# Kernel optimization log

Hardware: AMD Instinct MI355X
Metric: run time of the kernel (lower is better)

The kernel has to match this reference:

```python
import jax, jax.numpy as jnp
import numpy as np

H = 16  # num_heads (from init_kwargs)


def setup_inputs() -> dict:
    key = jax.random.key(0)
    ks = jax.random.split(key, 12)
    B, S, E = 4, 1024, 1024
    inp = {
        "query": jax.random.normal(ks[0], (B, S, E), jnp.float32),
        "key": jax.random.normal(ks[1], (B, S, E), jnp.float32),
        "value": jax.random.normal(ks[2], (B, S, E), jnp.float32),
        "mask": jax.random.randint(ks[3], (B, S, S), 0, 2, jnp.int32),
        # nn.Linear params: y = x @ W.T + b
        "Wq": jax.random.normal(ks[4], (E, E), jnp.float32) * 0.02,
        "bq": jnp.zeros((E,), jnp.float32),
        "Wk": jax.random.normal(ks[5], (E, E), jnp.float32) * 0.02,
        "bk": jnp.zeros((E,), jnp.float32),
        "Wv": jax.random.normal(ks[6], (E, E), jnp.float32) * 0.02,
        "bv": jnp.zeros((E,), jnp.float32),
        "Wo": jax.random.normal(ks[7], (E, E), jnp.float32) * 0.02,
        "bo": jnp.zeros((E,), jnp.float32),
    }
    return inp


def reference(query, key, value, mask, Wq, bq, Wk, bk, Wv, bv, Wo, bo):
    # Dropout treated as identity (eval mode) for a deterministic baseline.
    B, Sq, E = query.shape
    Sk = key.shape[1]
    D = E // H
    scale = jnp.sqrt(jnp.float32(D))

    Q = (query @ Wq.T + bq).reshape(B, Sq, H, D).transpose(0, 2, 1, 3)  # bhqd
    K = (key @ Wk.T + bk).reshape(B, Sk, H, D).transpose(0, 2, 1, 3)    # bhkd
    V = (value @ Wv.T + bv).reshape(B, Sk, H, D).transpose(0, 2, 1, 3)  # bhkd

    scores = jnp.einsum("bhqd,bhkd->bhqk", Q, K) / scale
    scores = jnp.where(mask[:, None, :, :] == 0, jnp.float32(-1e9), scores)
    attn = jax.nn.softmax(scores, axis=-1)  # [B,H,Sq,Sk]

    ctx = jnp.einsum("bhqk,bhkd->bhqd", attn, V)
    ctx = ctx.transpose(0, 2, 1, 3).reshape(B, Sq, E)
    out = ctx @ Wo.T + bo
    attn_avg = attn.mean(axis=1)  # [B,Sq,Sk]
    return out, attn_avg
```

## Files before the change

kernel.cpp:

```cpp
#include <hip/hip_runtime.h>
#include <hip/hip_bf16.h>
#include <stdint.h>

#define BATCH 4
#define SEQ   1024
#define EMB   1024
#define NH    16
#define HD    64

typedef short s8v __attribute__((ext_vector_type(8)));
typedef float f4v __attribute__((ext_vector_type(4)));

__device__ __forceinline__ uint16_t f2bf(float f) {
    __hip_bfloat16 h = __float2bfloat16(f);
    return *reinterpret_cast<uint16_t*>(&h);
}
__device__ __forceinline__ short bfraw(float f) {
    __hip_bfloat16 h = __float2bfloat16(f);
    return *reinterpret_cast<short*>(&h);
}
__device__ __forceinline__ s8v cvt8(const float* p) {
    float4 a = *(const float4*)p;
    float4 b = *(const float4*)(p + 4);
    s8v r;
    r[0] = bfraw(a.x); r[1] = bfraw(a.y); r[2] = bfraw(a.z); r[3] = bfraw(a.w);
    r[4] = bfraw(b.x); r[5] = bfraw(b.y); r[6] = bfraw(b.z); r[7] = bfraw(b.w);
    return r;
}

__global__ __launch_bounds__(256) void pack_mask(
        const int* __restrict__ mask, unsigned long long* __restrict__ Mb64)
{
    const size_t gid = (size_t)blockIdx.x * 256 + threadIdx.x;
    const unsigned long long bal = __ballot(mask[gid] != 0);
    if ((threadIdx.x & 63) == 0) Mb64[gid >> 6] = bal;
}

__global__ __launch_bounds__(256) void cvt_all(
        const float* __restrict__ W0, const float* __restrict__ W1,
        const float* __restrict__ W2, const float* __restrict__ W3,
        const float* __restrict__ X0, const float* __restrict__ X1,
        const float* __restrict__ X2,
        uint16_t* __restrict__ Wdst, uint16_t* __restrict__ Xq,
        uint16_t* __restrict__ Xk, uint16_t* __restrict__ Xv)
{
    const int y = blockIdx.y;
    const size_t off = ((size_t)blockIdx.x * 256 + threadIdx.x) * 8;
    if (y < 4) {
        if (blockIdx.x >= 512) return;
        const float* s = (y == 0) ? W0 : (y == 1) ? W1 : (y == 2) ? W2 : W3;
        *(s8v*)(Wdst + (size_t)y * EMB * EMB + off) = cvt8(s + off);
    } else {
        const float* s = (y == 4) ? X0 : (y == 5) ? X1 : X2;
        uint16_t*    d = (y == 4) ? Xq : (y == 5) ? Xk : Xv;
        *(s8v*)(d + off) = cvt8(s + off);
    }
}

__global__ __launch_bounds__(512, 2) void gemm3(
        const uint16_t* __restrict__ X0, const uint16_t* __restrict__ W0,
        const float* __restrict__ b0, void* __restrict__ o0, int sc0, float ss0,
        const uint16_t* __restrict__ X1, const uint16_t* __restrict__ W1,
        const float* __restrict__ b1, void* __restrict__ o1, int sc1, float ss1,
        const uint16_t* __restrict__ X2, const uint16_t* __restrict__ W2,
        const float* __restrict__ b2, void* __restrict__ o2, int sc2, float ss2)
{
    __shared__ __attribute__((aligned(16))) uint16_t As[128][40];
    __shared__ __attribute__((aligned(16))) uint16_t Bs[128][40];

    const int z = blockIdx.z;
    const uint16_t* Xb   = (z == 0) ? X0 : (z == 1) ? X1 : X2;
    const uint16_t* Wb   = (z == 0) ? W0 : (z == 1) ? W1 : W2;
    const float*    bias = (z == 0) ? b0 : (z == 1) ? b1 : b2;
    void*           outv = (z == 0) ? o0 : (z == 1) ? o1 : o2;
    const int     scatter = (z == 0) ? sc0 : (z == 1) ? sc1 : sc2;
    const float   scale   = (z == 0) ? ss0 : (z == 1) ? ss1 : ss2;

    const int t    = threadIdx.x;
    const int lane = t & 63;
    const int w    = t >> 6;
    const int wm = w & 1;
    const int wn = w >> 1;
    const int m0 = blockIdx.y * 128;
    const int n0 = blockIdx.x * 128;
    const int ar = lane & 15;
    const int aq = lane >> 4;

    const int srow = t >> 2;
    const int scol = (t & 3) * 8;

    const uint16_t* gA = Xb + (size_t)(m0 + srow) * EMB + scol;
    const uint16_t* gB = Wb + (size_t)(n0 + srow) * EMB + scol;

    f4v acc[4][2];
    #pragma unroll
    for (int i = 0; i < 4; ++i)
        #pragma unroll
        for (int j = 0; j < 2; ++j) acc[i][j] = (f4v){0.f, 0.f, 0.f, 0.f};

    s8v ra = *(const s8v*)gA;
    s8v rb = *(const s8v*)gB;

    for (int k0 = 0; k0 < EMB; k0 += 32) {
        __syncthreads();
        *(s8v*)&As[srow][scol] = ra;
        *(s8v*)&Bs[srow][scol] = rb;
        const int kn = (k0 + 32) & (EMB - 1);
        ra = *(const s8v*)(gA + kn);
        rb = *(const s8v*)(gB + kn);
        __syncthreads();

        s8v af[4], bf[2];
        #pragma unroll
        for (int i = 0; i < 4; ++i)
            af[i] = *(const s8v*)&As[wm * 64 + i * 16 + ar][aq * 8];
        #pragma unroll
        for (int j = 0; j < 2; ++j)
            bf[j] = *(const s8v*)&Bs[wn * 32 + j * 16 + ar][aq * 8];
        #pragma unroll
        for (int i = 0; i < 4; ++i)
            #pragma unroll
            for (int j = 0; j < 2; ++j)
                acc[i][j] = __builtin_amdgcn_mfma_f32_16x16x32_bf16(af[i], bf[j], acc[i][j], 0, 0, 0);
    }

    #pragma unroll
    for (int i = 0; i < 4; ++i) {
        const int crow = m0 + wm * 64 + i * 16 + aq * 4;
        #pragma unroll
        for (int j = 0; j < 2; ++j) {
            const int n = n0 + wn * 32 + j * 16 + ar;
            const float bv = bias[n];
            #pragma unroll
            for (int r = 0; r < 4; ++r) {
                const int m = crow + r;
                const float v = (acc[i][j][r] + bv) * scale;
                if (scatter == 1) {
                    size_t idx = (size_t)(((m >> 10) * NH + (n >> 6)) * SEQ + (m & 1023)) * HD + (n & 63);
                    ((uint16_t*)outv)[idx] = f2bf(v);
                } else if (scatter == 2) {
                    size_t idx = (size_t)(((m >> 10) * NH + (n >> 6)) * HD + (n & 63)) * SEQ + (m & 1023);
                    ((uint16_t*)outv)[idx] = f2bf(v);
                } else {
                    ((float*)outv)[(size_t)m * EMB + n] = v;
                }
            }
        }
    }
}

__global__ __launch_bounds__(256, 4) void flash_ctx(
        const uint16_t* __restrict__ Qb, const uint16_t* __restrict__ Kb,
        const uint16_t* __restrict__ Vt, const uint32_t* __restrict__ Mb,
        uint16_t* __restrict__ ctx, float* __restrict__ linv_out)
{
    __shared__ uint32_t Ml[4][16][33];
    __shared__ __attribute__((aligned(16))) uint16_t Pt[4][2][16][56];

    const int t = threadIdx.x;
    const int w = t >> 6, lane = t & 63;
    const int ar = lane & 15, aq = lane >> 4;

    const int id   = blockIdx.x;
    const int xcd  = id & 7;
    const int rest = id >> 3;
    const int bh   = xcd * 8 + (rest & 7);
    const int qt   = (rest >> 3) * 4 + w;
    const int b = bh >> 4, h = bh & 15;
    const size_t hb = ((size_t)(b * NH + h)) * SEQ * HD;

    {
        const uint32_t* src = Mb + (((size_t)b * SEQ + qt * 16) << 5);
        uint4 m0 = *(const uint4*)(src + lane * 8);
        uint4 m1 = *(const uint4*)(src + lane * 8 + 4);
        const int pr = (lane * 8) >> 5, pc = (lane * 8) & 31;
        Ml[w][pr][pc + 0] = m0.x; Ml[w][pr][pc + 1] = m0.y;
        Ml[w][pr][pc + 2] = m0.z; Ml[w][pr][pc + 3] = m0.w;
        Ml[w][pr][pc + 4] = m1.x; Ml[w][pr][pc + 5] = m1.y;
        Ml[w][pr][pc + 6] = m1.z; Ml[w][pr][pc + 7] = m1.w;
    }

    const uint16_t* qp = Qb + hb + (size_t)(qt * 16 + ar) * HD + aq * 8;
    const s8v a0 = *(const s8v*)qp;
    const s8v a1 = *(const s8v*)(qp + 32);

    const uint16_t* kbase = Kb + hb + (size_t)ar * HD + aq * 8;
    const uint16_t* vbase = Vt + hb + (size_t)ar * SEQ + aq * 8;

    f4v OA0 = {0.f,0.f,0.f,0.f}, OA1 = OA0, OA2 = OA0, OA3 = OA0;
    f4v OB0 = OA0, OB1 = OA0, OB2 = OA0, OB3 = OA0;
    float lsA[4] = {0.f, 0.f, 0.f, 0.f};
    float lsB[4] = {0.f, 0.f, 0.f, 0.f};

    for (int ci = 0; ci < 16; ++ci) {
        const int cA = ci * 2, cB = ci * 2 + 1;
        const int kcA = cA * 32, kcB = cB * 32;

        const uint16_t* kA = kbase + (size_t)kcA * HD;
        const uint16_t* kB = kbase + (size_t)kcB * HD;
        s8v Abl0 = *(const s8v*)kA,            Abh0 = *(const s8v*)(kA + 32);
        s8v Abl1 = *(const s8v*)(kA + 16*HD),  Abh1 = *(const s8v*)(kA + 16*HD + 32);
        s8v Bbl0 = *(const s8v*)kB,            Bbh0 = *(const s8v*)(kB + 32);
        s8v Bbl1 = *(const s8v*)(kB + 16*HD),  Bbh1 = *(const s8v*)(kB + 16*HD + 32);

        f4v z = {0.f,0.f,0.f,0.f};
        f4v sA0 = __builtin_amdgcn_mfma_f32_16x16x32_bf16(a0, Abl0, z, 0, 0, 0);
        sA0 = __builtin_amdgcn_mfma_f32_16x16x32_bf16(a1, Abh0, sA0, 0, 0, 0);
        f4v sA1 = __builtin_amdgcn_mfma_f32_16x16x32_bf16(a0, Abl1, z, 0, 0, 0);
        sA1 = __builtin_amdgcn_mfma_f32_16x16x32_bf16(a1, Abh1, sA1, 0, 0, 0);
        f4v sB0 = __builtin_amdgcn_mfma_f32_16x16x32_bf16(a0, Bbl0, z, 0, 0, 0);
        sB0 = __builtin_amdgcn_mfma_f32_16x16x32_bf16(a1, Bbh0, sB0, 0, 0, 0);
        f4v sB1 = __builtin_amdgcn_mfma_f32_16x16x32_bf16(a0, Bbl1, z, 0, 0, 0);
        sB1 = __builtin_amdgcn_mfma_f32_16x16x32_bf16(a1, Bbh1, sB1, 0, 0, 0);

        const uint16_t* vA = vbase + kcA;
        const uint16_t* vB = vbase + kcB;
        s8v Av0 = *(const s8v*)(vA);
        s8v Av1 = *(const s8v*)(vA + 16 * SEQ);
        s8v Av2 = *(const s8v*)(vA + 32 * SEQ);
        s8v Av3 = *(const s8v*)(vA + 48 * SEQ);
        s8v Bv0 = *(const s8v*)(vB);
        s8v Bv1 = *(const s8v*)(vB + 16 * SEQ);
        s8v Bv2 = *(const s8v*)(vB + 32 * SEQ);
        s8v Bv3 = *(const s8v*)(vB + 48 * SEQ);

        #pragma unroll
        for (int r = 0; r < 4; ++r) {
            const uint32_t mwA = Ml[w][aq * 4 + r][cA];
            const float e0 = ((mwA >> ar) & 1u)        ? __expf(sA0[r]) : 0.f;
            const float e1 = ((mwA >> (16 + ar)) & 1u) ? __expf(sA1[r]) : 0.f;
            lsA[r] += e0 + e1;
            Pt[w][0][aq * 4 + r][ar]      = f2bf(e0);
            Pt[w][0][aq * 4 + r][16 + ar] = f2bf(e1);
        }
        #pragma unroll
        for (int r = 0; r < 4; ++r) {
            const uint32_t mwB = Ml[w][aq * 4 + r][cB];
            const float e0 = ((mwB >> ar) & 1u)        ? __expf(sB0[r]) : 0.f;
            const float e1 = ((mwB >> (16 + ar)) & 1u) ? __expf(sB1[r]) : 0.f;
            lsB[r] += e0 + e1;
            Pt[w][1][aq * 4 + r][ar]      = f2bf(e0);
            Pt[w][1][aq * 4 + r][16 + ar] = f2bf(e1);
        }

        const s8v paA = *(const s8v*)&Pt[w][0][ar][aq * 8];
        OA0 = __builtin_amdgcn_mfma_f32_16x16x32_bf16(paA, Av0, OA0, 0, 0, 0);
        OA1 = __builtin_amdgcn_mfma_f32_16x16x32_bf16(paA, Av1, OA1, 0, 0, 0);
        OA2 = __builtin_amdgcn_mfma_f32_16x16x32_bf16(paA, Av2, OA2, 0, 0, 0);
        OA3 = __builtin_amdgcn_mfma_f32_16x16x32_bf16(paA, Av3, OA3, 0, 0, 0);
        const s8v paB = *(const s8v*)&Pt[w][1][ar][aq * 8];
        OB0 = __builtin_amdgcn_mfma_f32_16x16x32_bf16(paB, Bv0, OB0, 0, 0, 0);
        OB1 = __builtin_amdgcn_mfma_f32_16x16x32_bf16(paB, Bv1, OB1, 0, 0, 0);
        OB2 = __builtin_amdgcn_mfma_f32_16x16x32_bf16(paB, Bv2, OB2, 0, 0, 0);
        OB3 = __builtin_amdgcn_mfma_f32_16x16x32_bf16(paB, Bv3, OB3, 0, 0, 0);
    }

    float lsum[4];
    #pragma unroll
    for (int r = 0; r < 4; ++r) {
        OA0[r] += OB0[r]; OA1[r] += OB1[r];
        OA2[r] += OB2[r]; OA3[r] += OB3[r];
        lsum[r] = lsA[r] + lsB[r];
    }

    #pragma unroll
    for (int off = 1; off < 16; off <<= 1) {
        #pragma unroll
        for (int r = 0; r < 4; ++r) lsum[r] += __shfl_xor(lsum[r], off);
    }
    float inv[4];
    #pragma unroll
    for (int r = 0; r < 4; ++r) inv[r] = 1.0f / lsum[r];

    #pragma unroll
    for (int r = 0; r < 4; ++r) {
        const int q = qt * 16 + aq * 4 + r;
        uint16_t* cp = ctx + ((size_t)(b * SEQ + q) * NH + h) * HD + ar;
        cp[ 0] = f2bf(OA0[r] * inv[r]);
        cp[16] = f2bf(OA1[r] * inv[r]);
        cp[32] = f2bf(OA2[r] * inv[r]);
        cp[48] = f2bf(OA3[r] * inv[r]);
    }
    if (ar == 0) {
        #pragma unroll
        for (int r = 0; r < 4; ++r)
            linv_out[(size_t)(b * NH + h) * SEQ + qt * 16 + aq * 4 + r] = inv[r];
    }
}

__global__ __launch_bounds__(512, 4) void attn_avg(
        const uint16_t* __restrict__ Qb, const uint16_t* __restrict__ Kb,
        const uint32_t* __restrict__ Mb, const float* __restrict__ linv,
        float* __restrict__ attn_out)
{
    const int qt = blockIdx.x;
    const int b  = blockIdx.y >> 2;
    const int kq = blockIdx.y & 3;
    const int t = threadIdx.x;
    const int w = t >> 6, lane = t & 63;
    const int ar = lane & 15, aq = lane >> 4;
    const int k0 = kq * 256 + w * 32;

    uint32_t mw[4];
    #pragma unroll
    for (int r = 0; r < 4; ++r)
        mw[r] = Mb[(((size_t)b * SEQ + qt * 16 + aq * 4 + r) << 5) + (k0 >> 5)];

    float acc[8];
    #pragma unroll
    for (int j = 0; j < 8; ++j) acc[j] = 0.f;

    for (int h = 0; h < NH; ++h) {
        const size_t hb = ((size_t)(b * NH + h)) * SEQ * HD;
        const uint16_t* qp = Qb + hb + (size_t)(qt * 16 + ar) * HD + aq * 8;
        const s8v a0 = *(const s8v*)qp;
        const s8v a1 = *(const s8v*)(qp + 32);
        float fs[4];
        #pragma unroll
        for (int r = 0; r < 4; ++r)
            fs[r] = linv[(size_t)(b * NH + h) * SEQ + qt * 16 + aq * 4 + r] * 0.0625f;

        #pragma unroll
        for (int nt = 0; nt < 2; ++nt) {
            const uint16_t* kp = Kb + hb + (size_t)(k0 + nt * 16 + ar) * HD + aq * 8;
            s8v bl = *(const s8v*)kp, bh2 = *(const s8v*)(kp + 32);
            f4v z = {0.f,0.f,0.f,0.f};
            f4v s = __builtin_amdgcn_mfma_f32_16x16x32_bf16(a0, bl, z, 0, 0, 0);
            s = __builtin_amdgcn_mfma_f32_16x16x32_bf16(a1, bh2, s, 0, 0, 0);
            #pragma unroll
            for (int r = 0; r < 4; ++r) {
                const int bit = nt * 16 + ar;
                if ((mw[r] >> bit) & 1u) acc[r * 2 + nt] += __expf(s[r]) * fs[r];
            }
        }
    }

    #pragma unroll
    for (int r = 0; r < 4; ++r) {
        float* ap = attn_out + ((size_t)b * SEQ + qt * 16 + aq * 4 + r) * SEQ + k0 + ar;
        #pragma unroll
        for (int nt = 0; nt < 2; ++nt) ap[nt * 16] = acc[r * 2 + nt];
    }
}

extern "C" void kernel_launch(void* const* d_in, const int* in_sizes, int n_in,
                              void* d_out, int out_size, void* d_ws, size_t ws_size,
                              hipStream_t stream) {
    const float* q_in = (const float*)d_in[0];
    const float* k_in = (const float*)d_in[1];
    const float* v_in = (const float*)d_in[2];
    const int*   mask = (const int*)d_in[3];
    const float* Wq = (const float*)d_in[4];
    const float* bq = (const float*)d_in[5];
    const float* Wk = (const float*)d_in[6];
    const float* bk = (const float*)d_in[7];
    const float* Wv = (const float*)d_in[8];
    const float* bv = (const float*)d_in[9];
    const float* Wo = (const float*)d_in[10];
    const float* bo = (const float*)d_in[11];

    float* out      = (float*)d_out;
    float* attn_out = out + (size_t)BATCH * SEQ * EMB;

    const size_t qkv_elems = (size_t)BATCH * NH * SEQ * HD;
    uint16_t* Qb  = (uint16_t*)d_ws;
    uint16_t* Kb  = Qb + qkv_elems;
    uint16_t* Vt  = Kb + qkv_elems;
    uint16_t* ctx = Vt + qkv_elems;
    uint16_t* Wcb = ctx + (size_t)BATCH * SEQ * EMB;
    uint16_t* Wqb = Wcb;
    uint16_t* Wkb = Wcb + (size_t)EMB * EMB;
    uint16_t* Wvb = Wcb + 2 * (size_t)EMB * EMB;
    uint16_t* Wob = Wcb + 3 * (size_t)EMB * EMB;
    uint16_t* Xq  = Wcb + 4 * (size_t)EMB * EMB;
    uint16_t* Xk  = Xq + qkv_elems;
    uint16_t* Xv  = ctx;
    uint32_t* Mb32 = (uint32_t*)(Xk + qkv_elems);
    float*    linv = (float*)(Mb32 + (size_t)BATCH * SEQ * 32);

    pack_mask<<<dim3((BATCH * SEQ * SEQ) / 256), 256, 0, stream>>>(
        mask, (unsigned long long*)Mb32);
    cvt_all<<<dim3(2048, 7), 256, 0, stream>>>(Wq, Wk, Wv, Wo, q_in, k_in, v_in,
                                               Wcb, Xq, Xk, Xv);

    dim3 g3(EMB / 128, (BATCH * SEQ) / 128, 3);
    gemm3<<<g3, 512, 0, stream>>>(
        Xq, Wqb, bq, Qb, 1, 0.125f,
        Xk, Wkb, bk, Kb, 1, 1.0f,
        Xv, Wvb, bv, Vt, 2, 1.0f);

    flash_ctx<<<dim3(1024), 256, 0, stream>>>(Qb, Kb, Vt, Mb32, ctx, linv);
    attn_avg<<<dim3(SEQ / 16, BATCH * 4), 512, 0, stream>>>(Qb, Kb, Mb32, linv, attn_out);

    dim3 g1(EMB / 128, (BATCH * SEQ) / 128, 1);
    gemm3<<<g1, 512, 0, stream>>>(
        ctx, Wob, bo, out, 0, 1.0f,
        ctx, Wob, bo, out, 0, 1.0f,
        ctx, Wob, bo, out, 0, 1.0f);
}
```

Baseline: 408.6 us.

## Deepen GEMM K-tile and software-pipeline K/V loads in flash attention

The projection GEMM now stages a 64-wide K slice per iteration, with each thread loading two rows, which halves the number of barrier pairs. The next tile's global loads are issued after the LDS stores and fenced with a sched_barrier. The flash attention kernel replaces its two-chunk interleaved loop with a single-chunk body that double-buffers the K and V registers, prefetching the next chunk before the current compute. This drops the duplicate accumulators and halves the Pt buffer. The gain relies on hiding global load latency, at the cost of more registers and LDS in the GEMM.

Measured after the change: 442.1 us. 8.2% more time.

```diff
diff --git a/kernel.cpp b/kernel.cpp
--- a/kernel.cpp
+++ b/kernel.cpp
@@ -65,8 +65,8 @@
         const uint16_t* __restrict__ X2, const uint16_t* __restrict__ W2,
         const float* __restrict__ b2, void* __restrict__ o2, int sc2, float ss2)
 {
-    __shared__ __attribute__((aligned(16))) uint16_t As[128][40];
-    __shared__ __attribute__((aligned(16))) uint16_t Bs[128][40];
+    __shared__ __attribute__((aligned(16))) uint16_t As[128][72];
+    __shared__ __attribute__((aligned(16))) uint16_t Bs[128][72];
 
     const int z = blockIdx.z;
     const uint16_t* Xb   = (z == 0) ? X0 : (z == 1) ? X1 : X2;
@@ -86,8 +86,8 @@
     const int ar = lane & 15;
     const int aq = lane >> 4;
 
-    const int srow = t >> 2;
-    const int scol = (t & 3) * 8;
+    const int srow = t >> 3;
+    const int scol = (t & 7) * 8;
 
     const uint16_t* gA = Xb + (size_t)(m0 + srow) * EMB + scol;
     const uint16_t* gB = Wb + (size_t)(n0 + srow) * EMB + scol;
@@ -98,30 +98,41 @@
         #pragma unroll
         for (int j = 0; j < 2; ++j) acc[i][j] = (f4v){0.f, 0.f, 0.f, 0.f};
 
-    s8v ra = *(const s8v*)gA;
-    s8v rb = *(const s8v*)gB;
-
-    for (int k0 = 0; k0 < EMB; k0 += 32) {
+    s8v ra0 = *(const s8v*)gA;
+    s8v ra1 = *(const s8v*)(gA + 64 * EMB);
+    s8v rb0 = *(const s8v*)gB;
+    s8v rb1 = *(const s8v*)(gB + 64 * EMB);
+
+    for (int k0 = 0; k0 < EMB; k0 += 64) {
         __syncthreads();
-        *(s8v*)&As[srow][scol] = ra;
-        *(s8v*)&Bs[srow][scol] = rb;
-        const int kn = (k0 + 32) & (EMB - 1);
-        ra = *(const s8v*)(gA + kn);
-        rb = *(const s8v*)(gB + kn);
+        *(s8v*)&As[srow][scol]      = ra0;
+        *(s8v*)&As[srow + 64][scol] = ra1;
+        *(s8v*)&Bs[srow][scol]      = rb0;
+        *(s8v*)&Bs[srow + 64][scol] = rb1;
         __syncthreads();
 
-        s8v af[4], bf[2];
-        #pragma unroll
-        for (int i = 0; i < 4; ++i)
-            af[i] = *(const s8v*)&As[wm * 64 + i * 16 + ar][aq * 8];
-        #pragma unroll
-        for (int j = 0; j < 2; ++j)
-            bf[j] = *(const s8v*)&Bs[wn * 32 + j * 16 + ar][aq * 8];
-        #pragma unroll
-        for (int i = 0; i < 4; ++i)
+        const int kn = (k0 + 64) & (EMB - 1);
+        ra0 = *(const s8v*)(gA + kn);
+        ra1 = *(const s8v*)(gA + 64 * EMB + kn);
+        rb0 = *(const s8v*)(gB + kn);
+        rb1 = *(const s8v*)(gB + 64 * EMB + kn);
+        __builtin_amdgcn_sched_barrier(0);
+
+        #pragma unroll
+        for (int kk = 0; kk < 2; ++kk) {
+            s8v af[4], bf[2];
+            #pragma unroll
+            for (int i = 0; i < 4; ++i)
+                af[i] = *(const s8v*)&As[wm * 64 + i * 16 + ar][kk * 32 + aq * 8];
             #pragma unroll
             for (int j = 0; j < 2; ++j)
-                acc[i][j] = __builtin_amdgcn_mfma_f32_16x16x32_bf16(af[i], bf[j], acc[i][j], 0, 0, 0);
+                bf[j] = *(const s8v*)&Bs[wn * 32 + j * 16 + ar][kk * 32 + aq * 8];
+            #pragma unroll
+            for (int i = 0; i < 4; ++i)
+                #pragma unroll
+                for (int j = 0; j < 2; ++j)
+                    acc[i][j] = __builtin_amdgcn_mfma_f32_16x16x32_bf16(af[i], bf[j], acc[i][j], 0, 0, 0);
+        }
     }
 
     #pragma unroll
@@ -155,7 +166,7 @@
         uint16_t* __restrict__ ctx, float* __restrict__ linv_out)
 {
     __shared__ uint32_t Ml[4][16][33];
-    __shared__ __attribute__((aligned(16))) uint16_t Pt[4][2][16][56];
+    __shared__ __attribute__((aligned(16))) uint16_t Pt[4][16][56];
 
     const int t = threadIdx.x;
     const int w = t >> 6, lane = t & 63;
@@ -187,80 +198,59 @@
     const uint16_t* kbase = Kb + hb + (size_t)ar * HD + aq * 8;
     const uint16_t* vbase = Vt + hb + (size_t)ar * SEQ + aq * 8;
 
-    f4v OA0 = {0.f,0.f,0.f,0.f}, OA1 = OA0, OA2 = OA0, OA3 = OA0;
-    f4v OB0 = OA0, OB1 = OA0, OB2 = OA0, OB3 = OA0;
-    float lsA[4] = {0.f, 0.f, 0.f, 0.f};
-    float lsB[4] = {0.f, 0.f, 0.f, 0.f};
-
-    for (int ci = 0; ci < 16; ++ci) {
-        const int cA = ci * 2, cB = ci * 2 + 1;
-        const int kcA = cA * 32, kcB = cB * 32;
-
-        const uint16_t* kA = kbase + (size_t)kcA * HD;
-        const uint16_t* kB = kbase + (size_t)kcB * HD;
-        s8v Abl0 = *(const s8v*)kA,            Abh0 = *(const s8v*)(kA + 32);
-        s8v Abl1 = *(const s8v*)(kA + 16*HD),  Abh1 = *(const s8v*)(kA + 16*HD + 32);
-        s8v Bbl0 = *(const s8v*)kB,            Bbh0 = *(const s8v*)(kB + 32);
-        s8v Bbl1 = *(const s8v*)(kB + 16*HD),  Bbh1 = *(const s8v*)(kB + 16*HD + 32);
+    f4v O0 = {0.f,0.f,0.f,0.f}, O1 = O0, O2 = O0, O3 = O0;
+    float lsum[4] = {0.f, 0.f, 0.f, 0.f};
+
+    auto body = [&](int ci, s8v* curK, s8v* curV, s8v* nxtK, s8v* nxtV) {
+        const int kcn = ((ci + 1) & 31) * 32;
+        const uint16_t* kn = kbase + (size_t)kcn * HD;
+        const uint16_t* vn = vbase + kcn;
+        nxtK[0] = *(const s8v*)kn;
+        nxtK[1] = *(const s8v*)(kn + 32);
+        nxtK[2] = *(const s8v*)(kn + 16 * HD);
+        nxtK[3] = *(const s8v*)(kn + 16 * HD + 32);
+        nxtV[0] = *(const s8v*)vn;
+        nxtV[1] = *(const s8v*)(vn + 16 * SEQ);
+        nxtV[2] = *(const s8v*)(vn + 32 * SEQ);
+        nxtV[3] = *(const s8v*)(vn + 48 * SEQ);
+        __builtin_amdgcn_sched_barrier(0);
 
         f4v z = {0.f,0.f,0.f,0.f};
-        f4v sA0 = __builtin_amdgcn_mfma_f32_16x16x32_bf16(a0, Abl0, z, 0, 0, 0);
-        sA0 = __builtin_amdgcn_mfma_f32_16x16x32_bf16(a1, Abh0, sA0, 0, 0, 0);
-        f4v sA1 = __builtin_amdgcn_mfma_f32_16x16x32_bf16(a0, Abl1, z, 0, 0, 0);
-        sA1 = __builtin_amdgcn_mfma_f32_16x16x32_bf16(a1, Abh1, sA1, 0, 0, 0);
-        f4v sB0 = __builtin_amdgcn_mfma_f32_16x16x32_bf16(a0, Bbl0, z, 0, 0, 0);
-        sB0 = __builtin_amdgcn_mfma_f32_16x16x32_bf16(a1, Bbh0, sB0, 0, 0, 0);
-        f4v sB1 = __builtin_amdgcn_mfma_f32_16x16x32_bf16(a0, Bbl1, z, 0, 0, 0);
-        sB1 = __builtin_amdgcn_mfma_f32_16x16x32_bf16(a1, Bbh1, sB1, 0, 0, 0);
-
-        const uint16_t* vA = vbase + kcA;
-        const uint16_t* vB = vbase + kcB;
-        s8v Av0 = *(const s8v*)(vA);
-        s8v Av1 = *(const s8v*)(vA + 16 * SEQ);
-        s8v Av2 = *(const s8v*)(vA + 32 * SEQ);
-        s8v Av3 = *(const s8v*)(vA + 48 * SEQ);
-        s8v Bv0 = *(const s8v*)(vB);
-        s8v Bv1 = *(const s8v*)(vB + 16 * SEQ);
-        s8v Bv2 = *(const s8v*)(vB + 32 * SEQ);
-        s8v Bv3 = *(const s8v*)(vB + 48 * SEQ);
+        f4v s0 = __builtin_amdgcn_mfma_f32_16x16x32_bf16(a0, curK[0], z, 0, 0, 0);
+        s0 = __builtin_amdgcn_mfma_f32_16x16x32_bf16(a1, curK[1], s0, 0, 0, 0);
+        f4v s1 = __builtin_amdgcn_mfma_f32_16x16x32_bf16(a0, curK[2], z, 0, 0, 0);
+        s1 = __builtin_amdgcn_mfma_f32_16x16x32_bf16(a1, curK[3], s1, 0, 0, 0);
 
         #pragma unroll
         for (int r = 0; r < 4; ++r) {
-            const uint32_t mwA = Ml[w][aq * 4 + r][cA];
-            const float e0 = ((mwA >> ar) & 1u)        ? __expf(sA0[r]) : 0.f;
-            const float e1 = ((mwA >> (16 + ar)) & 1u) ? __expf(sA1[r]) : 0.f;
-            lsA[r] += e0 + e1;
-            Pt[w][0][aq * 4 + r][ar]      = f2bf(e0);
-            Pt[w][0][aq * 4 + r][16 + ar] = f2bf(e1);
+            const uint32_t mw = Ml[w][aq * 4 + r][ci];
+            const float e0 = ((mw >> ar) & 1u)        ? __expf(s0[r]) : 0.f;
+            const float e1 = ((mw >> (16 + ar)) & 1u) ? __expf(s1[r]) : 0.f;
+            lsum[r] += e0 + e1;
+            Pt[w][aq * 4 + r][ar]      = f2bf(e0);
+            Pt[w][aq * 4 + r][16 + ar] = f2bf(e1);
         }
-        #pragma unroll
-        for (int r = 0; r < 4; ++r) {
-            const uint32_t mwB = Ml[w][aq * 4 + r][cB];
-            const float e0 = ((mwB >> ar) & 1u)        ? __expf(sB0[r]) : 0.f;
-            const float e1 = ((mwB >> (16 + ar)) & 1u) ? __expf(sB1[r]) : 0.f;
-            lsB[r] += e0 + e1;
-            Pt[w][1][aq * 4 + r][ar]      = f2bf(e0);
-            Pt[w][1][aq * 4 + r][16 + ar] = f2bf(e1);
-        }
-
-        const s8v paA = *(const s8v*)&Pt[w][0][ar][aq * 8];
-        OA0 = __builtin_amdgcn_mfma_f32_16x16x32_bf16(paA, Av0, OA0, 0, 0, 0);
-        OA1 = __builtin_amdgcn_mfma_f32_16x16x32_bf16(paA, Av1, OA1, 0, 0, 0);
-        OA2 = __builtin_amdgcn_mfma_f32_16x16x32_bf16(paA, Av2, OA2, 0, 0, 0);
-        OA3 = __builtin_amdgcn_mfma_f32_16x16x32_bf16(paA, Av3, OA3, 0, 0, 0);
-        const s8v paB = *(const s8v*)&Pt[w][1][ar][aq * 8];
-        OB0 = __builtin_amdgcn_mfma_f32_16x16x32_bf16(paB, Bv0, OB0, 0, 0, 0);
-        OB1 = __builtin_amdgcn_mfma_f32_16x16x32_bf16(paB, Bv1, OB1, 0, 0, 0);
-        OB2 = __builtin_amdgcn_mfma_f32_16x16x32_bf16(paB, Bv2, OB2, 0, 0, 0);
-        OB3 = __builtin_amdgcn_mfma_f32_16x16x32_bf16(paB, Bv3, OB3, 0, 0, 0);
-    }
-
-    float lsum[4];
-    #pragma unroll
-    for (int r = 0; r < 4; ++r) {
-        OA0[r] += OB0[r]; OA1[r] += OB1[r];
-        OA2[r] += OB2[r]; OA3[r] += OB3[r];
-        lsum[r] = lsA[r] + lsB[r];
+
+        const s8v pa = *(const s8v*)&Pt[w][ar][aq * 8];
+        O0 = __builtin_amdgcn_mfma_f32_16x16x32_bf16(pa, curV[0], O0, 0, 0, 0);
+        O1 = __builtin_amdgcn_mfma_f32_16x16x32_bf16(pa, curV[1], O1, 0, 0, 0);
+        O2 = __builtin_amdgcn_mfma_f32_16x16x32_bf16(pa, curV[2], O2, 0, 0, 0);
+        O3 = __builtin_amdgcn_mfma_f32_16x16x32_bf16(pa, curV[3], O3, 0, 0, 0);
+    };
+
+    s8v KA[4], VA[4], KB[4], VB[4];
+    KA[0] = *(const s8v*)kbase;
+    KA[1] = *(const s8v*)(kbase + 32);
+    KA[2] = *(const s8v*)(kbase + 16 * HD);
+    KA[3] = *(const s8v*)(kbase + 16 * HD + 32);
+    VA[0] = *(const s8v*)vbase;
+    VA[1] = *(const s8v*)(vbase + 16 * SEQ);
+    VA[2] = *(const s8v*)(vbase + 32 * SEQ);
+    VA[3] = *(const s8v*)(vbase + 48 * SEQ);
+
+    for (int ci = 0; ci < 32; ci += 2) {
+        body(ci,     KA, VA, KB, VB);
+        body(ci + 1, KB, VB, KA, VA);
     }
 
     #pragma unroll
@@ -276,10 +266,10 @@
     for (int r = 0; r < 4; ++r) {
         const int q = qt * 16 + aq * 4 + r;
         uint16_t* cp = ctx + ((size_t)(b * SEQ + q) * NH + h) * HD + ar;
-        cp[ 0] = f2bf(OA0[r] * inv[r]);
-        cp[16] = f2bf(OA1[r] * inv[r]);
-        cp[32] = f2bf(OA2[r] * inv[r]);
-        cp[48] = f2bf(OA3[r] * inv[r]);
+        cp[ 0] = f2bf(O0[r] * inv[r]);
+        cp[16] = f2bf(O1[r] * inv[r]);
+        cp[32] = f2bf(O2[r] * inv[r]);
+        cp[48] = f2bf(O3[r] * inv[r]);
     }
     if (ar == 0) {
         #pragma unroll
```
